# Optimization experiments

Hardware: AMD Instinct MI355X
Metric: run time of the kernel (lower is better)

## Reference

```python
import jax, jax.numpy as jnp
import numpy as np

EPS = 1e-4

@jax.custom_vjp
def bin_active(x):
    # BinActive: sign forward, straight-through (hard-tanh) backward
    return jnp.sign(x)

def _ba_fwd(x):
    return jnp.sign(x), x

def _ba_bwd(x, g):
    return (g * (jnp.abs(x) <= 1.0).astype(g.dtype),)

bin_active.defvjp(_ba_fwd, _ba_bwd)

def norm_bin(x):
    # per-node mean/std (torch .std is unbiased, ddof=1) then binarize
    x = x - jnp.mean(x, axis=1, keepdims=True)
    x = x / (jnp.std(x, axis=1, ddof=1, keepdims=True) + EPS)
    return bin_active(x)

def bin_weight(W):
    # XNOR-style weight binarization: per-output-row scale * sign(W)
    alpha = jnp.mean(jnp.abs(W), axis=1, keepdims=True)
    return alpha * jnp.sign(W)

def bi_sage_conv(x_src, x_tgt, edge_index, W_l, W_r, b):
    # mean-aggregate source messages onto targets, then two binarized linears
    src, dst = edge_index[0], edge_index[1]
    n_tgt = x_tgt.shape[0]
    msg = x_src[src]                                             # [E, F] gather
    agg = jax.ops.segment_sum(msg, dst, num_segments=n_tgt)       # [n_tgt, F]
    cnt = jax.ops.segment_sum(jnp.ones((src.shape[0],), x_src.dtype), dst,
                              num_segments=n_tgt)
    agg = agg / jnp.maximum(cnt, 1.0)[:, None]
    out = agg @ bin_weight(W_l).T + x_tgt @ bin_weight(W_r).T + b
    return out


def setup_inputs() -> dict:
    key = jax.random.key(0)
    ks = jax.random.split(key, 10)
    N0, N1, B = 292864, 11264, 1024
    F_IN, F_HID, F_OUT = 602, 256, 41
    E1, E2 = 281600, 10240
    x = jax.random.normal(ks[0], (N0, F_IN), dtype=jnp.float32)
    # bipartite edges: row0 = source idx in [0, n_src), row1 = target idx in [0, n_tgt)
    ei1 = jnp.stack([jax.random.randint(ks[1], (E1,), 0, N0),
                     jax.random.randint(ks[2], (E1,), 0, N1)]).astype(jnp.int64)
    ei2 = jnp.stack([jax.random.randint(ks[3], (E2,), 0, N1),
                     jax.random.randint(ks[4], (E2,), 0, B)]).astype(jnp.int64)
    s1 = 0.1
    return {
        "x": x,
        "edge_index1": ei1,
        "edge_index2": ei2,
        "n1": N1,
        "n_batch": B,
        "W1_l": s1 * jax.random.normal(ks[5], (F_HID, F_IN), dtype=jnp.float32),
        "W1_r": s1 * jax.random.normal(ks[6], (F_HID, F_IN), dtype=jnp.float32),
        "b1": jnp.zeros((F_HID,), jnp.float32),
        "W2_l": s1 * jax.random.normal(ks[7], (F_OUT, F_HID), dtype=jnp.float32),
        "W2_r": s1 * jax.random.normal(ks[8], (F_OUT, F_HID), dtype=jnp.float32),
        "b2": jnp.zeros((F_OUT,), jnp.float32),
    }


def reference(x, edge_index1, edge_index2, n1, n_batch,
              W1_l, W1_r, b1, W2_l, W2_r, b2):
    # layer 1
    x_t = x[:n1]
    h = bi_sage_conv(norm_bin(x), norm_bin(x_t), edge_index1, W1_l, W1_r, b1)
    h = jax.nn.relu(h)  # dropout p=0.0 -> identity
    # layer 2
    h_t = h[:n_batch]
    out = bi_sage_conv(norm_bin(h), norm_bin(h_t), edge_index2, W2_l, W2_r, b2)
    return jax.nn.log_softmax(out, axis=-1)
```

## Files before the change

kernel.cpp:

```cpp
#include <hip/hip_runtime.h>
#include <hip/hip_bf16.h>
#include <cstdint>
#include <cstddef>

#define CDIV(a,b) (((a)+(b)-1)/(b))

using bf16x8 = __attribute__((ext_vector_type(8))) short;
using f32x4  = __attribute__((ext_vector_type(4))) float;

struct __align__(8) F4 { float x, y, z, w; };
struct __align__(8) F2 { float x, y; };

__device__ __forceinline__ unsigned short sgn_bf16(float s){
  return (s > 0.f) ? 0x3F80u : ((s < 0.f) ? 0xBF80u : 0u);
}

__device__ __forceinline__ int colX(int k){
  int w = k >> 5, b = k & 31;
  if (w < 16){
    int g = w >> 3, wr = w & 7;
    int j = wr >> 1, half = wr & 1;
    return 256*g + 4*(32*half + b) + j;
  }
  int j = w - 16;
  int c = 512 + 4*b + j;
  return (c < 602) ? c : -1;
}
__device__ __forceinline__ int colH(int k){
  int w = k >> 5, b = k & 31;
  int j = w >> 1, half = w & 1;
  return 4*(32*half + b) + j;
}

__global__ void prep_all(const float* __restrict__ W1l, const float* __restrict__ W1r,
                         const float* __restrict__ W2l, const float* __restrict__ W2r,
                         float* __restrict__ aL, float* __restrict__ aR,
                         float* __restrict__ a2L, float* __restrict__ a2R,
                         int* __restrict__ degB, int ndeg,
                         unsigned short* __restrict__ bsgn){
  int r = blockIdx.x;
  if (r < 594){
    const float* wr; float* dst; int K;
    if (r < 256){ wr = W1l + (size_t)r*602; dst = aL + r; K = 602; }
    else if (r < 512){ int q = r-256; wr = W1r + (size_t)q*602; dst = aR + q; K = 602; }
    else if (r < 553){ int q = r-512; wr = W2l + (size_t)q*256; dst = a2L + q; K = 256; }
    else { int q = r-553; wr = W2r + (size_t)q*256; dst = a2R + q; K = 256; }
    float s = 0.f;
    for (int k = threadIdx.x; k < K; k += blockDim.x) s += fabsf(wr[k]);
    #pragma unroll
    for (int off = 32; off; off >>= 1) s += __shfl_xor(s, off);
    __shared__ float red[4];
    int wid = threadIdx.x >> 6, lane = threadIdx.x & 63;
    if (lane == 0) red[wid] = s;
    __syncthreads();
    if (threadIdx.x == 0) *dst = (red[0]+red[1]+red[2]+red[3]) / (float)K;
  } else if (r < 642){
    int i = (r - 594)*256 + threadIdx.x;
    if (i < ndeg) degB[i] = 0;
  } else {
    int idx = (r - 642)*256 + threadIdx.x;
    if (idx < 256*1280){
      int o = idx / 1280, k = idx - o*1280;
      float v = 0.f;
      if (k < 640){ int c = colX(k);       if (c >= 0) v = W1l[(size_t)o*602 + c]; }
      else        { int c = colX(k - 640); if (c >= 0) v = W1r[(size_t)o*602 + c]; }
      bsgn[idx] = sgn_bf16(v);
    }
  }
}

__global__ void packx_count(const float* __restrict__ X, uint32_t* __restrict__ P, int nrows,
                            const int* __restrict__ d1, int E1, int* __restrict__ deg1,
                            const int* __restrict__ d2, int E2, int* __restrict__ deg2,
                            int packBlocks){
  if ((int)blockIdx.x >= packBlocks){
    int e = ((int)blockIdx.x - packBlocks)*blockDim.x + threadIdx.x;
    if (e < E1) atomicAdd(&deg1[d1[e]], 1);
    else if (e < E1 + E2) atomicAdd(&deg2[d2[e - E1]], 1);
    return;
  }
  const int row = blockIdx.x*4 + (threadIdx.x >> 6);
  const int lane = threadIdx.x & 63;
  if (row >= nrows) return;
  const float* xr = X + (size_t)row * 602;
  F4 v0 = *(const F4*)&xr[4*lane];
  F4 v1 = *(const F4*)&xr[256 + 4*lane];
  F4 v2 = {0.f,0.f,0.f,0.f};
  if (lane < 22) v2 = *(const F4*)&xr[512 + 4*lane];
  else if (lane == 22){ F2 t = *(const F2*)&xr[600]; v2.x = t.x; v2.y = t.y; }
  float s = v0.x+v0.y+v0.z+v0.w + v1.x+v1.y+v1.z+v1.w + v2.x+v2.y+v2.z+v2.w;
  #pragma unroll
  for (int off = 32; off; off >>= 1) s += __shfl_xor(s, off);
  const float mean = s / 602.f;
  uint32_t wpos[20], wneg[20];
  {
    float d0 = v0.x - mean, d1v = v0.y - mean, d2v = v0.z - mean, d3 = v0.w - mean;
    unsigned long long b0 = __ballot(d0 > 0.f), b1 = __ballot(d1v > 0.f),
                       b2 = __ballot(d2v > 0.f), b3 = __ballot(d3 > 0.f);
    wpos[0]=(uint32_t)b0; wpos[1]=(uint32_t)(b0>>32); wpos[2]=(uint32_t)b1; wpos[3]=(uint32_t)(b1>>32);
    wpos[4]=(uint32_t)b2; wpos[5]=(uint32_t)(b2>>32); wpos[6]=(uint32_t)b3; wpos[7]=(uint32_t)(b3>>32);
    b0 = __ballot(d0 < 0.f); b1 = __ballot(d1v < 0.f); b2 = __ballot(d2v < 0.f); b3 = __ballot(d3 < 0.f);
    wneg[0]=(uint32_t)b0; wneg[1]=(uint32_t)(b0>>32); wneg[2]=(uint32_t)b1; wneg[3]=(uint32_t)(b1>>32);
    wneg[4]=(uint32_t)b2; wneg[5]=(uint32_t)(b2>>32); wneg[6]=(uint32_t)b3; wneg[7]=(uint32_t)(b3>>32);
  }
  {
    float d0 = v1.x - mean, d1v = v1.y - mean, d2v = v1.z - mean, d3 = v1.w - mean;
    unsigned long long b0 = __ballot(d0 > 0.f), b1 = __ballot(d1v > 0.f),
                       b2 = __ballot(d2v > 0.f), b3 = __ballot(d3 > 0.f);
    wpos[8]=(uint32_t)b0; wpos[9]=(uint32_t)(b0>>32); wpos[10]=(uint32_t)b1; wpos[11]=(uint32_t)(b1>>32);
    wpos[12]=(uint32_t)b2; wpos[13]=(uint32_t)(b2>>32); wpos[14]=(uint32_t)b3; wpos[15]=(uint32_t)(b3>>32);
    b0 = __ballot(d0 < 0.f); b1 = __ballot(d1v < 0.f); b2 = __ballot(d2v < 0.f); b3 = __ballot(d3 < 0.f);
    wneg[8]=(uint32_t)b0; wneg[9]=(uint32_t)(b0>>32); wneg[10]=(uint32_t)b1; wneg[11]=(uint32_t)(b1>>32);
    wneg[12]=(uint32_t)b2; wneg[13]=(uint32_t)(b2>>32); wneg[14]=(uint32_t)b3; wneg[15]=(uint32_t)(b3>>32);
  }
  {
    int base = 4*lane;
    float d0 = v2.x - mean, d1v = v2.y - mean, d2v = v2.z - mean, d3 = v2.w - mean;
    wpos[16] = (uint32_t)__ballot((base+0 < 90) && (d0 > 0.f));
    wpos[17] = (uint32_t)__ballot((base+1 < 90) && (d1v > 0.f));
    wpos[18] = (uint32_t)__ballot((base+2 < 90) && (d2v > 0.f));
    wpos[19] = (uint32_t)__ballot((base+3 < 90) && (d3 > 0.f));
    wneg[16] = (uint32_t)__ballot((base+0 < 90) && (d0 < 0.f));
    wneg[17] = (uint32_t)__ballot((base+1 < 90) && (d1v < 0.f));
    wneg[18] = (uint32_t)__ballot((base+2 < 90) && (d2v < 0.f));
    wneg[19] = (uint32_t)__ballot((base+3 < 90) && (d3 < 0.f));
  }
  if (lane == 0){
    uint32_t* pr = P + (size_t)row * 40;
    #pragma unroll
    for (int q = 0; q < 5; ++q){
      uint4 a; a.x = wpos[4*q]; a.y = wpos[4*q+1]; a.z = wpos[4*q+2]; a.w = wpos[4*q+3];
      *(uint4*)&pr[4*q] = a;
      uint4 b; b.x = wneg[4*q]; b.y = wneg[4*q+1]; b.z = wneg[4*q+2]; b.w = wneg[4*q+3];
      *(uint4*)&pr[20 + 4*q] = b;
    }
  }
}

__global__ void scan_bcat(const int* __restrict__ deg1, int* __restrict__ rs1, int* __restrict__ cur1, int n1,
                          const int* __restrict__ deg2, int* __restrict__ rs2, int* __restrict__ cur2, int n2,
                          const float* __restrict__ W2l, const float* __restrict__ W2r,
                          const float* __restrict__ a2L, const float* __restrict__ a2R,
                          float* __restrict__ Bcat2){
  if (blockIdx.x < 2){
    const int* deg = blockIdx.x ? deg2 : deg1;
    int* rs  = blockIdx.x ? rs2  : rs1;
    int* cur = blockIdx.x ? cur2 : cur1;
    int n    = blockIdx.x ? n2   : n1;
    __shared__ int partial[1024];
    int tid = threadIdx.x;
    int per = CDIV(n, 1024);
    int begin = tid*per; if (begin > n) begin = n;
    int end = begin + per; if (end > n) end = n;
    int s = 0;
    for (int i = begin; i < end; ++i) s += deg[i];
    partial[tid] = s;
    __syncthreads();
    for (int off = 1; off < 1024; off <<= 1){
      int add = (tid >= off) ? partial[tid-off] : 0;
      __syncthreads();
      partial[tid] += add;
      __syncthreads();
    }
    int prefix = (tid == 0) ? 0 : partial[tid-1];
    for (int i = begin; i < end; ++i){ rs[i] = prefix; cur[i] = prefix; prefix += deg[i]; }
    if (tid == 1023) rs[n] = prefix;
  } else {
    int idx = (blockIdx.x - 2)*1024 + threadIdx.x;
    if (idx < 512*41){
      int o = idx % 41, k = idx / 41;
      int c = (k < 256) ? colH(k) : colH(k - 256);
      float w = (k < 256) ? W2l[(size_t)o*256 + c] : W2r[(size_t)o*256 + c];
      float a = (k < 256) ? a2L[o] : a2R[o];
      float sg = (w > 0.f) ? 1.f : ((w < 0.f) ? -1.f : 0.f);
      Bcat2[idx] = a * sg;
    }
  }
}

__global__ void fill_both(const int* __restrict__ s1, const int* __restrict__ d1, int E1,
                          int* __restrict__ cur1, int* __restrict__ esrc1,
                          const int* __restrict__ s2, const int* __restrict__ d2, int E2,
                          int* __restrict__ cur2, int* __restrict__ esrc2){
  int e = blockIdx.x*blockDim.x + threadIdx.x;
  if (e < E1){
    int p = atomicAdd(&cur1[d1[e]], 1);
    esrc1[p] = s1[e];
  } else if (e < E1 + E2){
    int q = e - E1;
    int p = atomicAdd(&cur2[d2[q]], 1);
    esrc2[p] = s2[q];
  }
}

template<int WUSED, int HALF, int STRIDE, int KPAD>
__global__ void aggregate_bf16(const uint32_t* __restrict__ packed,
                               const int* __restrict__ rs, const int* __restrict__ esrc,
                               unsigned short* __restrict__ S, float* __restrict__ invdeg){
  const int t = blockIdx.x;
  const int lane = threadIdx.x;
  const int s0 = rs[t], s1 = rs[t+1];
  uint32_t p[8] = {0,0,0,0,0,0,0,0};
  uint32_t n[8] = {0,0,0,0,0,0,0,0};
  if (lane < WUSED){
    for (int e = s0; e < s1; ++e){
      const uint32_t* pr = packed + (size_t)esrc[e] * STRIDE;
      uint32_t wp = pr[lane];
      uint32_t wn = pr[HALF + lane];
      #pragma unroll
      for (int b = 0; b < 8; ++b){
        p[b] += (wp >> b) & 0x01010101u;
        n[b] += (wn >> b) & 0x01010101u;
      }
    }
  }
  if (lane == 0){
    int deg = s1 - s0;
    invdeg[t] = 1.f / (float)(deg > 0 ? deg : 1);
  }
  if (lane < WUSED){
    unsigned short* sr = S + (size_t)t * KPAD;
    #pragma unroll
    for (int b = 0; b < 8; ++b){
      #pragma unroll
      for (int k = 0; k < 4; ++k){
        int col = 32*lane + b + 8*k;
        int cnt = (int)((p[b] >> (8*k)) & 0xFF) - (int)((n[b] >> (8*k)) & 0xFF);
        float f = (float)cnt;
        sr[col] = (unsigned short)(__float_as_uint(f) >> 16);
      }
    }
  }
}

__global__ __launch_bounds__(256) void gemm1_mfma(
    const unsigned short* __restrict__ Sx, const uint32_t* __restrict__ packedX,
    const unsigned short* __restrict__ bsgn, const float* __restrict__ invdeg,
    const float* __restrict__ aL, const float* __restrict__ aR,
    const float* __restrict__ bias, float* __restrict__ H){
  __shared__ __align__(16) unsigned short As[64][40];
  __shared__ __align__(16) unsigned short Bs[128][40];
  const int tid = threadIdx.x;
  const int lane = tid & 63, wid = tid >> 6;
  const int wm = wid & 1, wn = wid >> 1;
  const int m0 = blockIdx.y * 64, n0 = blockIdx.x * 128;
  const int sArow = tid >> 2, sAk = (tid & 3) * 8;
  const int sBcol = tid >> 1, sBk = (tid & 1) * 16;
  const int frow = lane & 15, fk = (lane >> 4) * 8;
  f32x4 acc1[2][4], acc2[2][4];
  #pragma unroll
  for (int i = 0; i < 2; ++i)
    #pragma unroll
    for (int j = 0; j < 4; ++j){ f32x4 z = {0.f,0.f,0.f,0.f}; acc1[i][j] = z; acc2[i][j] = z; }

  const unsigned short* SxRow = Sx + (size_t)(m0 + sArow) * 640;
  const uint32_t* pxRow = packedX + (size_t)(m0 + sArow) * 40;
  const unsigned short* bsgnRow = bsgn + (size_t)(n0 + sBcol) * 1280;

  for (int kc = 0; kc < 640; kc += 32){
    *(bf16x8*)&As[sArow][sAk] = *(const bf16x8*)&SxRow[kc + sAk];
    *(bf16x8*)&Bs[sBcol][sBk]     = *(const bf16x8*)&bsgnRow[kc + sBk];
    *(bf16x8*)&Bs[sBcol][sBk + 8] = *(const bf16x8*)&bsgnRow[kc + sBk + 8];
    __syncthreads();
    bf16x8 a0 = *(bf16x8*)&As[wm*32 + frow][fk];
    bf16x8 a1 = *(bf16x8*)&As[wm*32 + 16 + frow][fk];
    #pragma unroll
    for (int nf = 0; nf < 4; ++nf){
      bf16x8 b = *(bf16x8*)&Bs[wn*64 + nf*16 + frow][fk];
      acc1[0][nf] = __builtin_amdgcn_mfma_f32_16x16x32_bf16(a0, b, acc1[0][nf], 0, 0, 0);
      acc1[1][nf] = __builtin_amdgcn_mfma_f32_16x16x32_bf16(a1, b, acc1[1][nf], 0, 0, 0);
    }
    __syncthreads();
  }
  for (int kc = 0; kc < 640; kc += 32){
    int w = kc >> 5;
    {
      uint32_t wp = pxRow[w];
      uint32_t wq = pxRow[20 + w];
      unsigned short tmp[8];
      #pragma unroll
      for (int j = 0; j < 8; ++j){
        int b_ = sAk + j;
        tmp[j] = ((wp >> b_) & 1) ? 0x3F80u : (((wq >> b_) & 1) ? 0xBF80u : 0u);
      }
      *(bf16x8*)&As[sArow][sAk] = *(bf16x8*)tmp;
    }
    *(bf16x8*)&Bs[sBcol][sBk]     = *(const bf16x8*)&bsgnRow[640 + kc + sBk];
    *(bf16x8*)&Bs[sBcol][sBk + 8] = *(const bf16x8*)&bsgnRow[640 + kc + sBk + 8];
    __syncthreads();
    bf16x8 a0 = *(bf16x8*)&As[wm*32 + frow][fk];
    bf16x8 a1 = *(bf16x8*)&As[wm*32 + 16 + frow][fk];
    #pragma unroll
    for (int nf = 0; nf < 4; ++nf){
      bf16x8 b = *(bf16x8*)&Bs[wn*64 + nf*16 + frow][fk];
      acc2[0][nf] = __builtin_amdgcn_mfma_f32_16x16x32_bf16(a0, b, acc2[0][nf], 0, 0, 0);
      acc2[1][nf] = __builtin_amdgcn_mfma_f32_16x16x32_bf16(a1, b, acc2[1][nf], 0, 0, 0);
    }
    __syncthreads();
  }
  #pragma unroll
  for (int nf = 0; nf < 4; ++nf){
    int gc = n0 + wn*64 + nf*16 + frow;
    float al = aL[gc], ar = aR[gc], bb = bias[gc];
    #pragma unroll
    for (int mf = 0; mf < 2; ++mf){
      #pragma unroll
      for (int reg = 0; reg < 4; ++reg){
        int gr = m0 + wm*32 + mf*16 + (lane >> 4)*4 + reg;
        float v = invdeg[gr]*al*acc1[mf][nf][reg] + ar*acc2[mf][nf][reg] + bb;
        H[(size_t)gr*256 + gc] = fmaxf(v, 0.f);
      }
    }
  }
}

__global__ void pack_h(const float* __restrict__ H, uint32_t* __restrict__ P, int nrows){
  const int row = blockIdx.x*4 + (threadIdx.x >> 6);
  const int lane = threadIdx.x & 63;
  if (row >= nrows) return;
  const float* hr = H + (size_t)row * 256;
  float4 v = *(const float4*)&hr[4*lane];
  float s = v.x + v.y + v.z + v.w;
  #pragma unroll
  for (int off = 32; off; off >>= 1) s += __shfl_xor(s, off);
  const float mean = s / 256.f;
  float d0 = v.x - mean, d1v = v.y - mean, d2v = v.z - mean, d3 = v.w - mean;
  uint32_t wpos[8], wneg[8];
  unsigned long long b0 = __ballot(d0 > 0.f), b1 = __ballot(d1v > 0.f),
                     b2 = __ballot(d2v > 0.f), b3 = __ballot(d3 > 0.f);
  wpos[0]=(uint32_t)b0; wpos[1]=(uint32_t)(b0>>32); wpos[2]=(uint32_t)b1; wpos[3]=(uint32_t)(b1>>32);
  wpos[4]=(uint32_t)b2; wpos[5]=(uint32_t)(b2>>32); wpos[6]=(uint32_t)b3; wpos[7]=(uint32_t)(b3>>32);
  b0 = __ballot(d0 < 0.f); b1 = __ballot(d1v < 0.f); b2 = __ballot(d2v < 0.f); b3 = __ballot(d3 < 0.f);
  wneg[0]=(uint32_t)b0; wneg[1]=(uint32_t)(b0>>32); wneg[2]=(uint32_t)b1; wneg[3]=(uint32_t)(b1>>32);
  wneg[4]=(uint32_t)b2; wneg[5]=(uint32_t)(b2>>32); wneg[6]=(uint32_t)b3; wneg[7]=(uint32_t)(b3>>32);
  if (lane == 0){
    uint32_t* pr = P + (size_t)row * 16;
    *(uint4*)&pr[0]  = make_uint4(wpos[0], wpos[1], wpos[2], wpos[3]);
    *(uint4*)&pr[4]  = make_uint4(wpos[4], wpos[5], wpos[6], wpos[7]);
    *(uint4*)&pr[8]  = make_uint4(wneg[0], wneg[1], wneg[2], wneg[3]);
    *(uint4*)&pr[12] = make_uint4(wneg[4], wneg[5], wneg[6], wneg[7]);
  }
}

__global__ void agg_gemm2(const uint32_t* __restrict__ packedH,
                          const int* __restrict__ rs, const int* __restrict__ esrc,
                          const float* __restrict__ Bcat2, const float* __restrict__ bias,
                          float* __restrict__ out){
  const int t = blockIdx.x;
  const int lane = threadIdx.x;
  __shared__ float av[512];
  const int s0 = rs[t], s1 = rs[t+1];
  uint32_t p[8] = {0,0,0,0,0,0,0,0};
  uint32_t n[8] = {0,0,0,0,0,0,0,0};
  if (lane < 8){
    for (int e = s0; e < s1; ++e){
      const uint32_t* pr = packedH + (size_t)esrc[e] * 16;
      uint32_t wp = pr[lane];
      uint32_t wn = pr[8 + lane];
      #pragma unroll
      for (int b = 0; b < 8; ++b){
        p[b] += (wp >> b) & 0x01010101u;
        n[b] += (wn >> b) & 0x01010101u;
      }
    }
    int deg = s1 - s0;
    float inv = 1.f / (float)(deg > 0 ? deg : 1);
    #pragma unroll
    for (int b = 0; b < 8; ++b){
      #pragma unroll
      for (int k = 0; k < 4; ++k){
        int col = 32*lane + b + 8*k;
        int cnt = (int)((p[b] >> (8*k)) & 0xFF) - (int)((n[b] >> (8*k)) & 0xFF);
        av[col] = (float)cnt * inv;
      }
    }
  }
  const uint32_t* pr = packedH + (size_t)t * 16;
  for (int k = lane; k < 256; k += 64){
    int w = k >> 5, b = k & 31;
    av[256 + k] = (float)((pr[w] >> b) & 1) - (float)((pr[8 + w] >> b) & 1);
  }
  __syncthreads();
  bool active = lane < 41;
  float acc = active ? bias[lane] : 0.f;
  for (int k = 0; k < 512; ++k){
    float bw = active ? Bcat2[k*41 + lane] : 0.f;
    acc += av[k] * bw;
  }
  float v = active ? acc : -INFINITY;
  float m = v;
  #pragma unroll
  for (int off = 32; off; off >>= 1) m = fmaxf(m, __shfl_xor(m, off));
  float e = active ? expf(v - m) : 0.f;
  float ssum = e;
  #pragma unroll
  for (int off = 32; off; off >>= 1) ssum += __shfl_xor(ssum, off);
  if (active) out[(size_t)t*41 + lane] = v - m - logf(ssum);
}

extern "C" void kernel_launch(void* const* d_in, const int* in_sizes, int n_in,
                              void* d_out, int out_size, void* d_ws, size_t ws_size,
                              hipStream_t stream){
  (void)n_in; (void)out_size; (void)ws_size;
  const float* x   = (const float*)d_in[0];
  const int*   ei1 = (const int*)d_in[1];
  const int*   ei2 = (const int*)d_in[2];
  const float* W1l = (const float*)d_in[5];
  const float* W1r = (const float*)d_in[6];
  const float* b1  = (const float*)d_in[7];
  const float* W2l = (const float*)d_in[8];
  const float* W2r = (const float*)d_in[9];
  const float* b2  = (const float*)d_in[10];
  float* out = (float*)d_out;

  const int FIN = 602, N1 = 11264, NB = 1024;
  const int N0 = in_sizes[0] / FIN;
  const int E1 = in_sizes[1] / 2;
  const int E2 = in_sizes[2] / 2;

  char* wsb = (char*)d_ws;
  size_t off = 0;
  auto carve = [&](size_t bytes)->void*{
    void* p = wsb + off;
    off = (off + bytes + 255) & ~(size_t)255;
    return p;
  };
  uint32_t* packedX = (uint32_t*)carve((size_t)N0*40*4);
  uint32_t* packedH = (uint32_t*)carve((size_t)N1*16*4);
  unsigned short* Sx = (unsigned short*)carve((size_t)N1*640*2);
  float* invdeg1 = (float*)carve((size_t)N1*4);
  float* h     = (float*)carve((size_t)N1*256*4);
  unsigned short* bsgn = (unsigned short*)carve((size_t)256*1280*2);
  float* Bcat2 = (float*)carve((size_t)512*41*4);
  float* aL  = (float*)carve(256*4);
  float* aR  = (float*)carve(256*4);
  float* a2L = (float*)carve(64*4);
  float* a2R = (float*)carve(64*4);
  int* degB  = (int*)carve((size_t)(N1+NB)*4);
  int* deg1  = degB;
  int* deg2  = degB + N1;
  int* rs1   = (int*)carve((size_t)(N1+1)*4);
  int* cur1  = (int*)carve((size_t)N1*4);
  int* esrc1 = (int*)carve((size_t)E1*4);
  int* rs2   = (int*)carve((size_t)(NB+1)*4);
  int* cur2  = (int*)carve((size_t)NB*4);
  int* esrc2 = (int*)carve((size_t)E2*4);

  const int packBlocks = CDIV(N0, 4);
  const int cntBlocks  = CDIV(E1 + E2, 256);

  prep_all<<<1922, 256, 0, stream>>>(W1l, W1r, W2l, W2r, aL, aR, a2L, a2R,
                                     degB, N1 + NB, bsgn);
  packx_count<<<packBlocks + cntBlocks, 256, 0, stream>>>(
      x, packedX, N0, ei1 + E1, E1, deg1, ei2 + E2, E2, deg2, packBlocks);
  scan_bcat<<<2 + CDIV(512*41, 1024), 1024, 0, stream>>>(
      deg1, rs1, cur1, N1, deg2, rs2, cur2, NB, W2l, W2r, a2L, a2R, Bcat2);
  fill_both<<<cntBlocks, 256, 0, stream>>>(ei1, ei1 + E1, E1, cur1, esrc1,
                                           ei2, ei2 + E2, E2, cur2, esrc2);
  aggregate_bf16<20,20,40,640><<<N1, 64, 0, stream>>>(packedX, rs1, esrc1, Sx, invdeg1);
  gemm1_mfma<<<dim3(2, 176), 256, 0, stream>>>(Sx, packedX, bsgn, invdeg1, aL, aR, b1, h);
  pack_h<<<CDIV(N1, 4), 256, 0, stream>>>(h, packedH, N1);
  agg_gemm2<<<NB, 64, 0, stream>>>(packedH, rs2, esrc2, Bcat2, b2, out);
}
```

Before: 309.9 us.

## Pack only referenced source rows and fuse layer-1 GEMM with hidden binarization

Adds a mask pass that marks x rows actually used, either as edge sources or as the first n1 target rows, so the binarize/pack kernel skips reading unused rows of the large 292864x602 input. It also fuses the layer-1 GEMM epilogue with the hidden-row normalize/sign packing. The GEMM tile becomes 32 rows by the full 256 columns and the result goes through shared memory, which removes the fp32 h round trip and the separate pack_h launch. The cost is one extra kernel launch with byte-scatter writes, and a GEMM grid with fewer, larger blocks that may lower occupancy.

Measured after the change: 282.0 us. 9.0% less time.

```diff
diff --git a/kernel.cpp b/kernel.cpp
--- a/kernel.cpp
+++ b/kernel.cpp
@@ -37,7 +37,8 @@
                          float* __restrict__ aL, float* __restrict__ aR,
                          float* __restrict__ a2L, float* __restrict__ a2R,
                          int* __restrict__ degB, int ndeg,
-                         unsigned short* __restrict__ bsgn){
+                         unsigned short* __restrict__ bsgn,
+                         unsigned char* __restrict__ mask, int n0, int n1){
   int r = blockIdx.x;
   if (r < 594){
     const float* wr; float* dst; int K;
@@ -57,7 +58,7 @@
   } else if (r < 642){
     int i = (r - 594)*256 + threadIdx.x;
     if (i < ndeg) degB[i] = 0;
-  } else {
+  } else if (r < 1922){
     int idx = (r - 642)*256 + threadIdx.x;
     if (idx < 256*1280){
       int o = idx / 1280, k = idx - o*1280;
@@ -66,22 +67,30 @@
       else        { int c = colX(k - 640); if (c >= 0) v = W1r[(size_t)o*602 + c]; }
       bsgn[idx] = sgn_bf16(v);
     }
-  }
-}
-
-__global__ void packx_count(const float* __restrict__ X, uint32_t* __restrict__ P, int nrows,
-                            const int* __restrict__ d1, int E1, int* __restrict__ deg1,
-                            const int* __restrict__ d2, int E2, int* __restrict__ deg2,
-                            int packBlocks){
-  if ((int)blockIdx.x >= packBlocks){
-    int e = ((int)blockIdx.x - packBlocks)*blockDim.x + threadIdx.x;
-    if (e < E1) atomicAdd(&deg1[d1[e]], 1);
-    else if (e < E1 + E2) atomicAdd(&deg2[d2[e - E1]], 1);
-    return;
-  }
+  } else {
+    int i = (r - 1922)*256 + threadIdx.x;
+    if (i < n0) mask[i] = (i < n1) ? 1 : 0;
+  }
+}
+
+__global__ void mark_count(const int* __restrict__ s1, const int* __restrict__ d1, int E1,
+                           unsigned char* __restrict__ mask, int* __restrict__ deg1,
+                           const int* __restrict__ d2, int E2, int* __restrict__ deg2){
+  int e = blockIdx.x*blockDim.x + threadIdx.x;
+  if (e < E1){
+    mask[s1[e]] = 1;
+    atomicAdd(&deg1[d1[e]], 1);
+  } else if (e < E1 + E2){
+    atomicAdd(&deg2[d2[e - E1]], 1);
+  }
+}
+
+__global__ void pack_masked(const float* __restrict__ X, uint32_t* __restrict__ P, int nrows,
+                            const unsigned char* __restrict__ mask){
   const int row = blockIdx.x*4 + (threadIdx.x >> 6);
   const int lane = threadIdx.x & 63;
   if (row >= nrows) return;
+  if (!mask[row]) return;
   const float* xr = X + (size_t)row * 602;
   F4 v0 = *(const F4*)&xr[4*lane];
   F4 v1 = *(const F4*)&xr[256 + 4*lane];
@@ -233,40 +242,44 @@
   }
 }
 
-__global__ __launch_bounds__(256) void gemm1_mfma(
+__global__ __launch_bounds__(256) void gemm1_fused(
     const unsigned short* __restrict__ Sx, const uint32_t* __restrict__ packedX,
     const unsigned short* __restrict__ bsgn, const float* __restrict__ invdeg,
     const float* __restrict__ aL, const float* __restrict__ aR,
-    const float* __restrict__ bias, float* __restrict__ H){
-  __shared__ __align__(16) unsigned short As[64][40];
-  __shared__ __align__(16) unsigned short Bs[128][40];
+    const float* __restrict__ bias, uint32_t* __restrict__ packedH){
+  __shared__ __align__(16) char smem[33792];
+  unsigned short (*As)[40] = (unsigned short (*)[40])smem;
+  unsigned short (*Bs)[40] = (unsigned short (*)[40])(smem + 32*40*2);
+  float (*Hs)[264] = (float (*)[264])smem;
+
   const int tid = threadIdx.x;
   const int lane = tid & 63, wid = tid >> 6;
-  const int wm = wid & 1, wn = wid >> 1;
-  const int m0 = blockIdx.y * 64, n0 = blockIdx.x * 128;
-  const int sArow = tid >> 2, sAk = (tid & 3) * 8;
-  const int sBcol = tid >> 1, sBk = (tid & 1) * 16;
+  const int m0 = blockIdx.x * 32;
   const int frow = lane & 15, fk = (lane >> 4) * 8;
+  const int sRow = tid >> 3, sK = (tid & 7) * 4;
+
   f32x4 acc1[2][4], acc2[2][4];
   #pragma unroll
   for (int i = 0; i < 2; ++i)
     #pragma unroll
     for (int j = 0; j < 4; ++j){ f32x4 z = {0.f,0.f,0.f,0.f}; acc1[i][j] = z; acc2[i][j] = z; }
 
-  const unsigned short* SxRow = Sx + (size_t)(m0 + sArow) * 640;
-  const uint32_t* pxRow = packedX + (size_t)(m0 + sArow) * 40;
-  const unsigned short* bsgnRow = bsgn + (size_t)(n0 + sBcol) * 1280;
+  const unsigned short* SxRow = Sx + (size_t)(m0 + sRow) * 640;
+  const uint32_t* pxRow = packedX + (size_t)(m0 + sRow) * 40;
+  const unsigned short* bsgnCol = bsgn + (size_t)tid * 1280;
 
   for (int kc = 0; kc < 640; kc += 32){
-    *(bf16x8*)&As[sArow][sAk] = *(const bf16x8*)&SxRow[kc + sAk];
-    *(bf16x8*)&Bs[sBcol][sBk]     = *(const bf16x8*)&bsgnRow[kc + sBk];
-    *(bf16x8*)&Bs[sBcol][sBk + 8] = *(const bf16x8*)&bsgnRow[kc + sBk + 8];
-    __syncthreads();
-    bf16x8 a0 = *(bf16x8*)&As[wm*32 + frow][fk];
-    bf16x8 a1 = *(bf16x8*)&As[wm*32 + 16 + frow][fk];
+    *(uint2*)&As[sRow][sK] = *(const uint2*)&SxRow[kc + sK];
+    *(bf16x8*)&Bs[tid][0]  = *(const bf16x8*)&bsgnCol[kc];
+    *(bf16x8*)&Bs[tid][8]  = *(const bf16x8*)&bsgnCol[kc + 8];
+    *(bf16x8*)&Bs[tid][16] = *(const bf16x8*)&bsgnCol[kc + 16];
+    *(bf16x8*)&Bs[tid][24] = *(const bf16x8*)&bsgnCol[kc + 24];
+    __syncthreads();
+    bf16x8 a0 = *(bf16x8*)&As[frow][fk];
+    bf16x8 a1 = *(bf16x8*)&As[16 + frow][fk];
     #pragma unroll
     for (int nf = 0; nf < 4; ++nf){
-      bf16x8 b = *(bf16x8*)&Bs[wn*64 + nf*16 + frow][fk];
+      bf16x8 b = *(bf16x8*)&Bs[wid*64 + nf*16 + frow][fk];
       acc1[0][nf] = __builtin_amdgcn_mfma_f32_16x16x32_bf16(a0, b, acc1[0][nf], 0, 0, 0);
       acc1[1][nf] = __builtin_amdgcn_mfma_f32_16x16x32_bf16(a1, b, acc1[1][nf], 0, 0, 0);
     }
@@ -277,68 +290,69 @@
     {
       uint32_t wp = pxRow[w];
       uint32_t wq = pxRow[20 + w];
-      unsigned short tmp[8];
-      #pragma unroll
-      for (int j = 0; j < 8; ++j){
-        int b_ = sAk + j;
-        tmp[j] = ((wp >> b_) & 1) ? 0x3F80u : (((wq >> b_) & 1) ? 0xBF80u : 0u);
-      }
-      *(bf16x8*)&As[sArow][sAk] = *(bf16x8*)tmp;
-    }
-    *(bf16x8*)&Bs[sBcol][sBk]     = *(const bf16x8*)&bsgnRow[640 + kc + sBk];
-    *(bf16x8*)&Bs[sBcol][sBk + 8] = *(const bf16x8*)&bsgnRow[640 + kc + sBk + 8];
-    __syncthreads();
-    bf16x8 a0 = *(bf16x8*)&As[wm*32 + frow][fk];
-    bf16x8 a1 = *(bf16x8*)&As[wm*32 + 16 + frow][fk];
+      union { unsigned short u[4]; uint2 v; } tmp;
+      #pragma unroll
+      for (int j = 0; j < 4; ++j){
+        int b_ = sK + j;
+        tmp.u[j] = ((wp >> b_) & 1) ? 0x3F80u : (((wq >> b_) & 1) ? 0xBF80u : 0u);
+      }
+      *(uint2*)&As[sRow][sK] = tmp.v;
+    }
+    *(bf16x8*)&Bs[tid][0]  = *(const bf16x8*)&bsgnCol[640 + kc];
+    *(bf16x8*)&Bs[tid][8]  = *(const bf16x8*)&bsgnCol[640 + kc + 8];
+    *(bf16x8*)&Bs[tid][16] = *(const bf16x8*)&bsgnCol[640 + kc + 16];
+    *(bf16x8*)&Bs[tid][24] = *(const bf16x8*)&bsgnCol[640 + kc + 24];
+    __syncthreads();
+    bf16x8 a0 = *(bf16x8*)&As[frow][fk];
+    bf16x8 a1 = *(bf16x8*)&As[16 + frow][fk];
     #pragma unroll
     for (int nf = 0; nf < 4; ++nf){
-      bf16x8 b = *(bf16x8*)&Bs[wn*64 + nf*16 + frow][fk];
+      bf16x8 b = *(bf16x8*)&Bs[wid*64 + nf*16 + frow][fk];
       acc2[0][nf] = __builtin_amdgcn_mfma_f32_16x16x32_bf16(a0, b, acc2[0][nf], 0, 0, 0);
       acc2[1][nf] = __builtin_amdgcn_mfma_f32_16x16x32_bf16(a1, b, acc2[1][nf], 0, 0, 0);
     }
     __syncthreads();
   }
+
   #pragma unroll
   for (int nf = 0; nf < 4; ++nf){
-    int gc = n0 + wn*64 + nf*16 + frow;
+    int gc = wid*64 + nf*16 + frow;
     float al = aL[gc], ar = aR[gc], bb = bias[gc];
     #pragma unroll
     for (int mf = 0; mf < 2; ++mf){
       #pragma unroll
       for (int reg = 0; reg < 4; ++reg){
-        int gr = m0 + wm*32 + mf*16 + (lane >> 4)*4 + reg;
-        float v = invdeg[gr]*al*acc1[mf][nf][reg] + ar*acc2[mf][nf][reg] + bb;
-        H[(size_t)gr*256 + gc] = fmaxf(v, 0.f);
-      }
-    }
-  }
-}
-
-__global__ void pack_h(const float* __restrict__ H, uint32_t* __restrict__ P, int nrows){
-  const int row = blockIdx.x*4 + (threadIdx.x >> 6);
-  const int lane = threadIdx.x & 63;
-  if (row >= nrows) return;
-  const float* hr = H + (size_t)row * 256;
-  float4 v = *(const float4*)&hr[4*lane];
-  float s = v.x + v.y + v.z + v.w;
-  #pragma unroll
-  for (int off = 32; off; off >>= 1) s += __shfl_xor(s, off);
-  const float mean = s / 256.f;
-  float d0 = v.x - mean, d1v = v.y - mean, d2v = v.z - mean, d3 = v.w - mean;
-  uint32_t wpos[8], wneg[8];
-  unsigned long long b0 = __ballot(d0 > 0.f), b1 = __ballot(d1v > 0.f),
-                     b2 = __ballot(d2v > 0.f), b3 = __ballot(d3 > 0.f);
-  wpos[0]=(uint32_t)b0; wpos[1]=(uint32_t)(b0>>32); wpos[2]=(uint32_t)b1; wpos[3]=(uint32_t)(b1>>32);
-  wpos[4]=(uint32_t)b2; wpos[5]=(uint32_t)(b2>>32); wpos[6]=(uint32_t)b3; wpos[7]=(uint32_t)(b3>>32);
-  b0 = __ballot(d0 < 0.f); b1 = __ballot(d1v < 0.f); b2 = __ballot(d2v < 0.f); b3 = __ballot(d3 < 0.f);
-  wneg[0]=(uint32_t)b0; wneg[1]=(uint32_t)(b0>>32); wneg[2]=(uint32_t)b1; wneg[3]=(uint32_t)(b1>>32);
-  wneg[4]=(uint32_t)b2; wneg[5]=(uint32_t)(b2>>32); wneg[6]=(uint32_t)b3; wneg[7]=(uint32_t)(b3>>32);
-  if (lane == 0){
-    uint32_t* pr = P + (size_t)row * 16;
-    *(uint4*)&pr[0]  = make_uint4(wpos[0], wpos[1], wpos[2], wpos[3]);
-    *(uint4*)&pr[4]  = make_uint4(wpos[4], wpos[5], wpos[6], wpos[7]);
-    *(uint4*)&pr[8]  = make_uint4(wneg[0], wneg[1], wneg[2], wneg[3]);
-    *(uint4*)&pr[12] = make_uint4(wneg[4], wneg[5], wneg[6], wneg[7]);
+        int lr = mf*16 + (lane >> 4)*4 + reg;
+        float v = invdeg[m0 + lr]*al*acc1[mf][nf][reg] + ar*acc2[mf][nf][reg] + bb;
+        Hs[lr][gc] = fmaxf(v, 0.f);
+      }
+    }
+  }
+  __syncthreads();
+
+  for (int r = 0; r < 8; ++r){
+    int row = wid*8 + r;
+    float4 v = *(const float4*)&Hs[row][4*lane];
+    float s = v.x + v.y + v.z + v.w;
+    #pragma unroll
+    for (int off = 32; off; off >>= 1) s += __shfl_xor(s, off);
+    float mean = s * (1.f/256.f);
+    float d0 = v.x - mean, d1v = v.y - mean, d2v = v.z - mean, d3 = v.w - mean;
+    unsigned long long b0 = __ballot(d0 > 0.f), b1 = __ballot(d1v > 0.f),
+                       b2 = __ballot(d2v > 0.f), b3 = __ballot(d3 > 0.f);
+    uint32_t wpos[8], wneg[8];
+    wpos[0]=(uint32_t)b0; wpos[1]=(uint32_t)(b0>>32); wpos[2]=(uint32_t)b1; wpos[3]=(uint32_t)(b1>>32);
+    wpos[4]=(uint32_t)b2; wpos[5]=(uint32_t)(b2>>32); wpos[6]=(uint32_t)b3; wpos[7]=(uint32_t)(b3>>32);
+    b0 = __ballot(d0 < 0.f); b1 = __ballot(d1v < 0.f); b2 = __ballot(d2v < 0.f); b3 = __ballot(d3 < 0.f);
+    wneg[0]=(uint32_t)b0; wneg[1]=(uint32_t)(b0>>32); wneg[2]=(uint32_t)b1; wneg[3]=(uint32_t)(b1>>32);
+    wneg[4]=(uint32_t)b2; wneg[5]=(uint32_t)(b2>>32); wneg[6]=(uint32_t)b3; wneg[7]=(uint32_t)(b3>>32);
+    if (lane == 0){
+      uint32_t* pr = packedH + (size_t)(m0 + row) * 16;
+      *(uint4*)&pr[0]  = make_uint4(wpos[0], wpos[1], wpos[2], wpos[3]);
+      *(uint4*)&pr[4]  = make_uint4(wpos[4], wpos[5], wpos[6], wpos[7]);
+      *(uint4*)&pr[8]  = make_uint4(wneg[0], wneg[1], wneg[2], wneg[3]);
+      *(uint4*)&pr[12] = make_uint4(wneg[4], wneg[5], wneg[6], wneg[7]);
+    }
   }
 }
 
@@ -429,13 +443,13 @@
   uint32_t* packedH = (uint32_t*)carve((size_t)N1*16*4);
   unsigned short* Sx = (unsigned short*)carve((size_t)N1*640*2);
   float* invdeg1 = (float*)carve((size_t)N1*4);
-  float* h     = (float*)carve((size_t)N1*256*4);
   unsigned short* bsgn = (unsigned short*)carve((size_t)256*1280*2);
   float* Bcat2 = (float*)carve((size_t)512*41*4);
   float* aL  = (float*)carve(256*4);
   float* aR  = (float*)carve(256*4);
   float* a2L = (float*)carve(64*4);
   float* a2R = (float*)carve(64*4);
+  unsigned char* mask = (unsigned char*)carve((size_t)N0);
   int* degB  = (int*)carve((size_t)(N1+NB)*4);
   int* deg1  = degB;
   int* deg2  = degB + N1;
@@ -446,19 +460,19 @@
   int* cur2  = (int*)carve((size_t)NB*4);
   int* esrc2 = (int*)carve((size_t)E2*4);
 
-  const int packBlocks = CDIV(N0, 4);
+  const int maskBlocks = CDIV(N0, 256);
   const int cntBlocks  = CDIV(E1 + E2, 256);
 
-  prep_all<<<1922, 256, 0, stream>>>(W1l, W1r, W2l, W2r, aL, aR, a2L, a2R,
-                                     degB, N1 + NB, bsgn);
-  packx_count<<<packBlocks + cntBlocks, 256, 0, stream>>>(
-      x, packedX, N0, ei1 + E1, E1, deg1, ei2 + E2, E2, deg2, packBlocks);
+  prep_all<<<1922 + maskBlocks, 256, 0, stream>>>(
+      W1l, W1r, W2l, W2r, aL, aR, a2L, a2R, degB, N1 + NB, bsgn, mask, N0, N1);
+  mark_count<<<cntBlocks, 256, 0, stream>>>(ei1, ei1 + E1, E1, mask, deg1,
+                                            ei2 + E2, E2, deg2);
+  pack_masked<<<CDIV(N0, 4), 256, 0, stream>>>(x, packedX, N0, mask);
   scan_bcat<<<2 + CDIV(512*41, 1024), 1024, 0, stream>>>(
       deg1, rs1, cur1, N1, deg2, rs2, cur2, NB, W2l, W2r, a2L, a2R, Bcat2);
   fill_both<<<cntBlocks, 256, 0, stream>>>(ei1, ei1 + E1, E1, cur1, esrc1,
                                            ei2, ei2 + E2, E2, cur2, esrc2);
   aggregate_bf16<20,20,40,640><<<N1, 64, 0, stream>>>(packedX, rs1, esrc1, Sx, invdeg1);
-  gemm1_mfma<<<dim3(2, 176), 256, 0, stream>>>(Sx, packedX, bsgn, invdeg1, aL, aR, b1, h);
-  pack_h<<<CDIV(N1, 4), 256, 0, stream>>>(h, packedH, N1);
+  gemm1_fused<<<N1/32, 256, 0, stream>>>(Sx, packedX, bsgn, invdeg1, aL, aR, b1, packedH);
   agg_gemm2<<<NB, 64, 0, stream>>>(packedH, rs2, esrc2, Bcat2, b2, out);
 }
```
